# Performance work log

Hardware: AMD Instinct MI355X
Metric: run time of the kernel (lower is better)

Reference implementation:

```python
import jax, jax.numpy as jnp
import numpy as np

N_NODES = 400000
NUM_GRAPHS = 2048
IN_FEAT = 256
DENSE = 128
N_HEADS = 8


def setup_inputs() -> dict:
    key = jax.random.key(0)
    k_h, k_seg, k_w1, k_b1, k_w2, k_b2 = jax.random.split(key, 6)
    h = jax.random.normal(k_h, (N_NODES, IN_FEAT), dtype=jnp.float32)
    segment_ids = jnp.sort(
        jax.random.randint(k_seg, (N_NODES,), 0, NUM_GRAPHS, dtype=jnp.int32))
    # Linear params (jax convention: x @ W + b)
    W1 = jax.random.normal(k_w1, (IN_FEAT, DENSE), dtype=jnp.float32) / np.sqrt(IN_FEAT)
    b1 = jax.random.normal(k_b1, (DENSE,), dtype=jnp.float32) * 0.01
    W2 = jax.random.normal(k_w2, (DENSE, N_HEADS), dtype=jnp.float32) / np.sqrt(DENSE)
    b2 = jax.random.normal(k_b2, (N_HEADS,), dtype=jnp.float32) * 0.01
    return {"h": h, "segment_ids": segment_ids, "W1": W1, "b1": b1,
            "W2": W2, "b2": b2, "num_graphs": NUM_GRAPHS}


def reference(h, segment_ids, W1, b1, W2, b2, num_graphs):
    # scores: fc2(tanh(fc1(h))) -> [N, n_heads]
    scores = jnp.tanh(h @ W1 + b1) @ W2 + b2
    # ragged (per-graph) softmax over nodes, per head (dgl.softmax_nodes)
    seg_max = jax.ops.segment_max(scores, segment_ids, num_segments=num_graphs)  # [G, H]
    ex = jnp.exp(scores - seg_max[segment_ids])                                  # [N, H]
    denom = jax.ops.segment_sum(ex, segment_ids, num_segments=num_graphs)        # [G, H]
    attn = ex / denom[segment_ids]                                               # [N, H]
    # mean over heads of per-head weighted segment sums == segment sum with
    # head-averaged weights (linearity), avoiding H separate ndata passes.
    w = attn.mean(axis=1)                                                         # [N]
    out = jax.ops.segment_sum(h * w[:, None], segment_ids, num_segments=num_graphs)  # [G, in_feat]
    return out
```

## Files before the change

kernel.cpp:

```cpp
#include <hip/hip_runtime.h>
#include <hip/hip_bf16.h>

#define IN_FEAT 256
#define DENSE   128
#define NHEADS  8
#define MAXN    328
#define LDA     264
#define LDT2    136

typedef __attribute__((ext_vector_type(8))) short bf16x8_t;
typedef __attribute__((ext_vector_type(4))) float f32x4_t;

__device__ __forceinline__ unsigned int f2bf(float f) {
  unsigned int u = __float_as_uint(f);
  u += 0x7fffu + ((u >> 16) & 1u);
  return u >> 16;
}

__device__ __forceinline__ unsigned int f2bf_hu(float f) {
  return (__float_as_uint(f) + 0x8000u) >> 16;
}

__device__ __forceinline__ float fast_tanh(float x) {
  float ax = fabsf(x);
  float e = __expf(-2.0f * ax);
  float t = (1.0f - e) / (1.0f + e);
  return copysignf(t, x);
}

__global__ void seg_offsets_kernel(const int* __restrict__ seg, int* __restrict__ offs,
                                   int N, int G) {
  int i = blockIdx.x * blockDim.x + threadIdx.x;
  if (i >= N) return;
  int s  = seg[i];
  int sp = (i == 0) ? -1 : seg[i - 1];
  for (int g = sp + 1; g <= s; ++g) offs[g] = i;
  if (i == N - 1) {
    for (int g = s + 1; g <= G; ++g) offs[g] = N;
  }
}

__global__ void w1_frag_kernel(const float* __restrict__ W1, unsigned int* __restrict__ w1f) {
  int t = blockIdx.x * blockDim.x + threadIdx.x;
  if (t >= 4096) return;
  int lane = t & 63;
  int fid  = t >> 6;
  int ct = fid & 1;
  int ks = (fid >> 1) & 7;
  int wv = fid >> 4;
  int col = wv * 32 + ct * 16 + (lane & 15);
  int k0  = ks * 32 + (lane >> 4) * 8;
  unsigned int p[4];
  #pragma unroll
  for (int jj = 0; jj < 4; ++jj) {
    unsigned int lo = f2bf(W1[(size_t)(k0 + 2 * jj) * DENSE + col]);
    unsigned int hi = f2bf(W1[(size_t)(k0 + 2 * jj + 1) * DENSE + col]);
    p[jj] = lo | (hi << 16);
  }
  *(uint4*)&w1f[(size_t)t * 4] = make_uint4(p[0], p[1], p[2], p[3]);
}

__global__ void w2_frag_kernel(const float* __restrict__ W2, unsigned int* __restrict__ w2f) {
  int t = threadIdx.x;
  if (t >= 256) return;
  int lane = t & 63, ks = t >> 6;
  int hd = lane & 15, q = lane >> 4;
  unsigned int p[4];
  #pragma unroll
  for (int jj = 0; jj < 4; ++jj) {
    int k0 = ks * 32 + q * 8 + 2 * jj;
    unsigned int lo = (hd < 8) ? f2bf(W2[k0 * NHEADS + hd]) : 0u;
    unsigned int hi = (hd < 8) ? f2bf(W2[(k0 + 1) * NHEADS + hd]) : 0u;
    p[jj] = lo | (hi << 16);
  }
  *(uint4*)&w2f[(size_t)t * 4] = make_uint4(p[0], p[1], p[2], p[3]);
}

__device__ __forceinline__ int lower_bound_dev(const int* __restrict__ seg, int N, int v) {
  int lo = 0, hi = N;
  while (lo < hi) {
    int mid = (lo + hi) >> 1;
    if (seg[mid] < v) lo = mid + 1; else hi = mid;
  }
  return lo;
}

__launch_bounds__(256, 3)
__global__ void scores_kernel(const float* __restrict__ h,
                              const unsigned int* __restrict__ w1f,
                              const unsigned int* __restrict__ w2f,
                              const float* __restrict__ b1,
                              const float* __restrict__ b2,
                              float* __restrict__ scores,
                              int N) {
  __shared__ short sU[64 * LDA];
  __shared__ float sB1[DENSE];
  __shared__ float sB2[NHEADS];

  const int tid  = threadIdx.x;
  const int row0 = blockIdx.x * 64;
  const int rem  = N - row0;
  const int mcnt = rem < 64 ? rem : 64;

  const int lane = tid & 63;
  const int wv   = tid >> 6;
  const int lr   = lane & 15;
  const int q    = lane >> 4;
  const int q8   = q * 8;
  const int pfr  = tid >> 6;
  const int pfc4 = (tid & 63) * 4;

  if (tid < DENSE)  sB1[tid] = b1[tid];
  if (tid < NHEADS) sB2[tid] = b2[tid];

  short* sA = sU;
  #pragma unroll
  for (int it = 0; it < 16; ++it) {
    int row = it * 4 + pfr;
    float4 v = make_float4(0.f, 0.f, 0.f, 0.f);
    if (row < mcnt) v = *(const float4*)(h + (size_t)(row0 + row) * IN_FEAT + pfc4);
    unsigned int p0 = f2bf_hu(v.x) | (f2bf_hu(v.y) << 16);
    unsigned int p1 = f2bf_hu(v.z) | (f2bf_hu(v.w) << 16);
    *(uint2*)&sA[row * LDA + pfc4] = make_uint2(p0, p1);
  }
  __syncthreads();

  f32x4_t acc[4][2];
  #pragma unroll
  for (int mt = 0; mt < 4; ++mt) {
    acc[mt][0] = (f32x4_t){0, 0, 0, 0};
    acc[mt][1] = (f32x4_t){0, 0, 0, 0};
  }
  const bf16x8_t* w1fv = (const bf16x8_t*)w1f;
  #pragma unroll
  for (int ks = 0; ks < 8; ++ks) {
    bf16x8_t a0 = *(const bf16x8_t*)&sA[( 0 + lr) * LDA + ks * 32 + q8];
    bf16x8_t a1 = *(const bf16x8_t*)&sA[(16 + lr) * LDA + ks * 32 + q8];
    bf16x8_t a2 = *(const bf16x8_t*)&sA[(32 + lr) * LDA + ks * 32 + q8];
    bf16x8_t a3 = *(const bf16x8_t*)&sA[(48 + lr) * LDA + ks * 32 + q8];
    int f0 = ((wv * 8 + ks) * 2) * 64 + lane;
    bf16x8_t wf0 = w1fv[f0];
    bf16x8_t wf1 = w1fv[f0 + 64];
    acc[0][0] = __builtin_amdgcn_mfma_f32_16x16x32_bf16(a0, wf0, acc[0][0], 0, 0, 0);
    acc[0][1] = __builtin_amdgcn_mfma_f32_16x16x32_bf16(a0, wf1, acc[0][1], 0, 0, 0);
    acc[1][0] = __builtin_amdgcn_mfma_f32_16x16x32_bf16(a1, wf0, acc[1][0], 0, 0, 0);
    acc[1][1] = __builtin_amdgcn_mfma_f32_16x16x32_bf16(a1, wf1, acc[1][1], 0, 0, 0);
    acc[2][0] = __builtin_amdgcn_mfma_f32_16x16x32_bf16(a2, wf0, acc[2][0], 0, 0, 0);
    acc[2][1] = __builtin_amdgcn_mfma_f32_16x16x32_bf16(a2, wf1, acc[2][1], 0, 0, 0);
    acc[3][0] = __builtin_amdgcn_mfma_f32_16x16x32_bf16(a3, wf0, acc[3][0], 0, 0, 0);
    acc[3][1] = __builtin_amdgcn_mfma_f32_16x16x32_bf16(a3, wf1, acc[3][1], 0, 0, 0);
  }

  {
    float bias0 = sB1[wv * 32 + lr];
    float bias1 = sB1[wv * 32 + 16 + lr];
    #pragma unroll
    for (int mt = 0; mt < 4; ++mt)
      #pragma unroll
      for (int r = 0; r < 4; ++r) {
        acc[mt][0][r] = fast_tanh(acc[mt][0][r] + bias0);
        acc[mt][1][r] = fast_tanh(acc[mt][1][r] + bias1);
      }
  }
  __syncthreads();

  short* sTb = sU;
  #pragma unroll
  for (int mt = 0; mt < 4; ++mt) {
    int rbase = mt * 16 + q * 4;
    #pragma unroll
    for (int r = 0; r < 4; ++r) {
      sTb[(rbase + r) * LDT2 + wv * 32 + lr]      = (short)f2bf(acc[mt][0][r]);
      sTb[(rbase + r) * LDT2 + wv * 32 + 16 + lr] = (short)f2bf(acc[mt][1][r]);
    }
  }
  __syncthreads();

  {
    const bf16x8_t* w2fv = (const bf16x8_t*)w2f;
    float bias = (lr < 8) ? sB2[lr] : 0.0f;
    f32x4_t c = {bias, bias, bias, bias};
    #pragma unroll
    for (int ks = 0; ks < 4; ++ks) {
      bf16x8_t at = *(const bf16x8_t*)&sTb[(wv * 16 + lr) * LDT2 + ks * 32 + q8];
      bf16x8_t wf = w2fv[ks * 64 + lane];
      c = __builtin_amdgcn_mfma_f32_16x16x32_bf16(at, wf, c, 0, 0, 0);
    }
    #pragma unroll
    for (int r = 0; r < 4; ++r) {
      int ridx = wv * 16 + q * 4 + r;
      if (lr < 8 && ridx < mcnt)
        scores[(size_t)(row0 + ridx) * NHEADS + lr] = c[r];
    }
  }
}

__launch_bounds__(256, 4)
__global__ void pool_kernel(const float* __restrict__ h,
                            const float* __restrict__ scores,
                            const int* __restrict__ seg,
                            const int* __restrict__ offs,
                            float* __restrict__ out,
                            int N) {
  __shared__ float sS[MAXN * NHEADS];
  __shared__ float sWgt[MAXN];
  __shared__ float sRed[256];
  __shared__ float sMax[NHEADS];
  __shared__ float sInvD[NHEADS];

  const int g   = blockIdx.x;
  const int tid = threadIdx.x;

  int start, end;
  if (offs != nullptr) {
    start = offs[g];
    end   = offs[g + 1];
  } else {
    start = lower_bound_dev(seg, N, g);
    end   = lower_bound_dev(seg, N, g + 1);
  }
  int n = end - start;
  if (n > MAXN) n = MAXN;

  if (n == 0) {
    out[(size_t)g * IN_FEAT + tid] = 0.0f;
    return;
  }

  {
    const float4* sp = (const float4*)(scores + (size_t)start * NHEADS);
    float4* dp = (float4*)sS;
    int nf4 = n * 2;
    for (int idx = tid; idx < nf4; idx += 256) dp[idx] = sp[idx];
  }
  __syncthreads();

  {
    const int hd = tid & 7, ch = tid >> 3;
    float m = -3.4e38f;
    for (int i = ch; i < n; i += 32) m = fmaxf(m, sS[i * NHEADS + hd]);
    sRed[tid] = m;
    __syncthreads();
    if (tid < NHEADS) {
      float mm = sRed[tid];
      #pragma unroll
      for (int j = 1; j < 32; ++j) mm = fmaxf(mm, sRed[j * 8 + tid]);
      sMax[tid] = mm;
    }
    __syncthreads();
    float mm = sMax[hd], ssum = 0.f;
    for (int i = ch; i < n; i += 32) {
      float e = __expf(sS[i * NHEADS + hd] - mm);
      sS[i * NHEADS + hd] = e;
      ssum += e;
    }
    sRed[tid] = ssum;
    __syncthreads();
    if (tid < NHEADS) {
      float d = 0.f;
      #pragma unroll
      for (int j = 0; j < 32; ++j) d += sRed[j * 8 + tid];
      sInvD[tid] = 1.0f / d;
    }
    __syncthreads();
    for (int i = tid; i < n; i += 256) {
      float w = 0.f;
      #pragma unroll
      for (int hd2 = 0; hd2 < NHEADS; ++hd2) w += sS[i * NHEADS + hd2] * sInvD[hd2];
      sWgt[i] = 0.125f * w;
    }
    __syncthreads();
  }

  {
    const float* hp = h + (size_t)start * IN_FEAT + tid;
    float a0 = 0.f, a1 = 0.f, a2 = 0.f, a3 = 0.f;
    int i = 0;
    for (; i + 4 <= n; i += 4) {
      a0 = fmaf(sWgt[i    ], hp[(size_t)(i    ) * IN_FEAT], a0);
      a1 = fmaf(sWgt[i + 1], hp[(size_t)(i + 1) * IN_FEAT], a1);
      a2 = fmaf(sWgt[i + 2], hp[(size_t)(i + 2) * IN_FEAT], a2);
      a3 = fmaf(sWgt[i + 3], hp[(size_t)(i + 3) * IN_FEAT], a3);
    }
    for (; i < n; ++i) a0 = fmaf(sWgt[i], hp[(size_t)i * IN_FEAT], a0);
    out[(size_t)g * IN_FEAT + tid] = (a0 + a1) + (a2 + a3);
  }
}

__launch_bounds__(256, 3)
__global__ void attn_pool_fused(const float* __restrict__ h,
                                const int* __restrict__ seg,
                                const int* __restrict__ offs,
                                const float* __restrict__ W1,
                                const float* __restrict__ b1,
                                const float* __restrict__ W2,
                                const float* __restrict__ b2,
                                float* __restrict__ out,
                                int N) {
  __shared__ short sA[64 * LDA];
  __shared__ float sScores[MAXN * NHEADS];
  __shared__ float sWgt[MAXN];
  __shared__ float sW2T[NHEADS * 132];
  __shared__ float sB1[DENSE];
  __shared__ float sB2[NHEADS];
  __shared__ float sRed[256];
  __shared__ float sMax[NHEADS];
  __shared__ float sInvD[NHEADS];

  const int g   = blockIdx.x;
  const int tid = threadIdx.x;

  int start, end;
  if (offs != nullptr) { start = offs[g]; end = offs[g + 1]; }
  else { start = lower_bound_dev(seg, N, g); end = lower_bound_dev(seg, N, g + 1); }
  int n = end - start;
  if (n > MAXN) n = MAXN;
  float* sT = (float*)sA;

  if (n == 0) {
    if (tid < IN_FEAT) out[(size_t)g * IN_FEAT + tid] = 0.0f;
    return;
  }

  for (int idx = tid; idx < DENSE * NHEADS; idx += 256) {
    int k = idx >> 3; int hd = idx & 7;
    sW2T[hd * 132 + k] = W2[idx];
  }
  if (tid < DENSE)  sB1[tid] = b1[tid];
  if (tid < NHEADS) sB2[tid] = b2[tid];

  const int lane = tid & 63;
  const int wv   = tid >> 6;
  const int lr   = lane & 15;
  const int q    = lane >> 4;
  bf16x8_t b1f[16];
  #pragma unroll
  for (int ct = 0; ct < 2; ++ct) {
    int colb = wv * 32 + ct * 16 + lr;
    #pragma unroll
    for (int ks = 0; ks < 8; ++ks) {
      bf16x8_t bb;
      #pragma unroll
      for (int j = 0; j < 8; ++j)
        bb[j] = (short)f2bf(W1[(ks * 32 + q * 8 + j) * DENSE + colb]);
      b1f[ct * 8 + ks] = bb;
    }
  }

  const int ntiles = (n + 63) >> 6;
  for (int t = 0; t < ntiles; ++t) {
    const int m0   = start + t * 64;
    const int rem  = n - t * 64;
    const int mcnt = rem < 64 ? rem : 64;
    __syncthreads();
    #pragma unroll
    for (int it = 0; it < 16; ++it) {
      int row = it * 4 + (tid >> 6);
      int f4  = tid & 63;
      float4 v = make_float4(0.f, 0.f, 0.f, 0.f);
      if (row < mcnt) v = *(const float4*)(h + (size_t)(m0 + row) * IN_FEAT + f4 * 4);
      unsigned int p0 = f2bf(v.x) | (f2bf(v.y) << 16);
      unsigned int p1 = f2bf(v.z) | (f2bf(v.w) << 16);
      *(uint2*)&sA[row * LDA + f4 * 4] = make_uint2(p0, p1);
    }
    __syncthreads();
    f32x4_t acc[4][2];
    #pragma unroll
    for (int mt = 0; mt < 4; ++mt) {
      acc[mt][0] = (f32x4_t){0, 0, 0, 0};
      acc[mt][1] = (f32x4_t){0, 0, 0, 0};
    }
    #pragma unroll
    for (int ks = 0; ks < 8; ++ks) {
      bf16x8_t a0 = *(const bf16x8_t*)&sA[( 0 + lr) * LDA + ks * 32 + q * 8];
      bf16x8_t a1 = *(const bf16x8_t*)&sA[(16 + lr) * LDA + ks * 32 + q * 8];
      bf16x8_t a2 = *(const bf16x8_t*)&sA[(32 + lr) * LDA + ks * 32 + q * 8];
      bf16x8_t a3 = *(const bf16x8_t*)&sA[(48 + lr) * LDA + ks * 32 + q * 8];
      acc[0][0] = __builtin_amdgcn_mfma_f32_16x16x32_bf16(a0, b1f[ks],     acc[0][0], 0, 0, 0);
      acc[0][1] = __builtin_amdgcn_mfma_f32_16x16x32_bf16(a0, b1f[8 + ks], acc[0][1], 0, 0, 0);
      acc[1][0] = __builtin_amdgcn_mfma_f32_16x16x32_bf16(a1, b1f[ks],     acc[1][0], 0, 0, 0);
      acc[1][1] = __builtin_amdgcn_mfma_f32_16x16x32_bf16(a1, b1f[8 + ks], acc[1][1], 0, 0, 0);
      acc[2][0] = __builtin_amdgcn_mfma_f32_16x16x32_bf16(a2, b1f[ks],     acc[2][0], 0, 0, 0);
      acc[2][1] = __builtin_amdgcn_mfma_f32_16x16x32_bf16(a2, b1f[8 + ks], acc[2][1], 0, 0, 0);
      acc[3][0] = __builtin_amdgcn_mfma_f32_16x16x32_bf16(a3, b1f[ks],     acc[3][0], 0, 0, 0);
      acc[3][1] = __builtin_amdgcn_mfma_f32_16x16x32_bf16(a3, b1f[8 + ks], acc[3][1], 0, 0, 0);
    }
    __syncthreads();
    #pragma unroll
    for (int mt = 0; mt < 4; ++mt) {
      int rbase = mt * 16 + q * 4;
      #pragma unroll
      for (int ct = 0; ct < 2; ++ct) {
        int col = wv * 32 + ct * 16 + lr;
        float bias = sB1[col];
        #pragma unroll
        for (int r = 0; r < 4; ++r)
          sT[(rbase + r) * 132 + col] = fast_tanh(acc[mt][ct][r] + bias);
      }
    }
    __syncthreads();
    {
      int i0 = tid >> 3;
      int hd = tid & 7;
      #pragma unroll
      for (int half = 0; half < 2; ++half) {
        int i = i0 + half * 32;
        if (i < mcnt) {
          float s = sB2[hd];
          #pragma unroll
          for (int k4 = 0; k4 < DENSE; k4 += 4) {
            float4 tv  = *(const float4*)&sT[i * 132 + k4];
            float4 wv2 = *(const float4*)&sW2T[hd * 132 + k4];
            s = fmaf(tv.x, wv2.x, s); s = fmaf(tv.y, wv2.y, s);
            s = fmaf(tv.z, wv2.z, s); s = fmaf(tv.w, wv2.w, s);
          }
          sScores[(t * 64 + i) * NHEADS + hd] = s;
        }
      }
    }
  }
  __syncthreads();

  {
    const int hd = tid & 7, ch = tid >> 3;
    float m = -3.4e38f;
    for (int i = ch; i < n; i += 32) m = fmaxf(m, sScores[i * NHEADS + hd]);
    sRed[tid] = m;
    __syncthreads();
    if (tid < NHEADS) {
      float mm = sRed[tid];
      #pragma unroll
      for (int j = 1; j < 32; ++j) mm = fmaxf(mm, sRed[j * 8 + tid]);
      sMax[tid] = mm;
    }
    __syncthreads();
    float mm = sMax[hd], ssum = 0.f;
    for (int i = ch; i < n; i += 32) {
      float e = __expf(sScores[i * NHEADS + hd] - mm);
      sScores[i * NHEADS + hd] = e;
      ssum += e;
    }
    sRed[tid] = ssum;
    __syncthreads();
    if (tid < NHEADS) {
      float d = 0.f;
      #pragma unroll
      for (int j = 0; j < 32; ++j) d += sRed[j * 8 + tid];
      sInvD[tid] = 1.0f / d;
    }
    __syncthreads();
    for (int i = tid; i < n; i += 256) {
      float w = 0.f;
      #pragma unroll
      for (int hd2 = 0; hd2 < NHEADS; ++hd2) w += sScores[i * NHEADS + hd2] * sInvD[hd2];
      sWgt[i] = 0.125f * w;
    }
    __syncthreads();
  }

  {
    int grp = tid >> 6;
    int c4  = lane << 2;
    float4 acc = make_float4(0.f, 0.f, 0.f, 0.f);
    for (int i = grp; i < n; i += 4) {
      float w = sWgt[i];
      float4 hv = *(const float4*)(h + (size_t)(start + i) * IN_FEAT + c4);
      acc.x = fmaf(w, hv.x, acc.x);
      acc.y = fmaf(w, hv.y, acc.y);
      acc.z = fmaf(w, hv.z, acc.z);
      acc.w = fmaf(w, hv.w, acc.w);
    }
    float* sPart = (float*)sA;
    *(float4*)&sPart[grp * IN_FEAT + c4] = acc;
    __syncthreads();
    {
      float o = 0.f;
      #pragma unroll
      for (int p = 0; p < 4; ++p) o += sPart[p * IN_FEAT + tid];
      out[(size_t)g * IN_FEAT + tid] = o;
    }
  }
}

extern "C" void kernel_launch(void* const* d_in, const int* in_sizes, int n_in,
                              void* d_out, int out_size, void* d_ws, size_t ws_size,
                              hipStream_t stream) {
  const float* h   = (const float*)d_in[0];
  const int*   seg = (const int*)d_in[1];
  const float* W1  = (const float*)d_in[2];
  const float* b1v = (const float*)d_in[3];
  const float* W2  = (const float*)d_in[4];
  const float* b2v = (const float*)d_in[5];
  float* out = (float*)d_out;
  const int N = in_sizes[0] / IN_FEAT;
  const int G = out_size / IN_FEAT;

  const size_t offs_bytes  = (size_t)(G + 1) * sizeof(int);
  const size_t w1f_off     = (offs_bytes + 255) & ~(size_t)255;
  const size_t w1f_bytes   = 4096 * 16;
  const size_t w2f_off     = w1f_off + w1f_bytes;
  const size_t w2f_bytes   = 256 * 16;
  const size_t scores_off  = (w2f_off + w2f_bytes + 255) & ~(size_t)255;
  const size_t scores_bytes= (size_t)N * NHEADS * sizeof(float);

  int* offs = nullptr;
  if (ws_size >= offs_bytes) {
    offs = (int*)d_ws;
    seg_offsets_kernel<<<(N + 255) / 256, 256, 0, stream>>>(seg, offs, N, G);
  }

  if (ws_size >= scores_off + scores_bytes) {
    unsigned int* w1f = (unsigned int*)((char*)d_ws + w1f_off);
    unsigned int* w2f = (unsigned int*)((char*)d_ws + w2f_off);
    float* scores = (float*)((char*)d_ws + scores_off);
    w1_frag_kernel<<<16, 256, 0, stream>>>(W1, w1f);
    w2_frag_kernel<<<1, 256, 0, stream>>>(W2, w2f);
    scores_kernel<<<(N + 63) / 64, 256, 0, stream>>>(h, w1f, w2f, b1v, b2v, scores, N);
    pool_kernel<<<G, 256, 0, stream>>>(h, scores, seg, offs, out, N);
  } else {
    attn_pool_fused<<<G, 256, 0, stream>>>(h, seg, offs, W1, b1v, W2, b2v, out, N);
  }
}
```

Measured before the change: 198.4 us.

## Fuse score computation and pooling into one pass with atomic segment accumulation

Replaces the separate scores and per-graph pool kernels with one kernel over 32-row tiles. Each tile computes the MLP scores, exponentiates them without subtracting the segment max, and accumulates per-head exp-weighted sums of the bf16-staged h rows into a global [G,H,F] buffer and a per-head denominator buffer using atomics. A small finalize kernel then normalises and averages over heads. The aim is to read h from HBM only once instead of twice. The cost is a memset of the accumulators, many float atomics, pooling on bf16-rounded h, and reliance on scores being small enough that exp does not overflow.

```diff
diff --git a/kernel.cpp b/kernel.cpp
--- a/kernel.cpp
+++ b/kernel.cpp
@@ -5,6 +5,7 @@
 #define DENSE   128
 #define NHEADS  8
 #define MAXN    328
+#define TILE    32
 #define LDA     264
 #define LDT2    136
 
@@ -19,6 +20,10 @@
 
 __device__ __forceinline__ unsigned int f2bf_hu(float f) {
   return (__float_as_uint(f) + 0x8000u) >> 16;
+}
+
+__device__ __forceinline__ float bf2f(short s) {
+  return __uint_as_float(((unsigned int)(unsigned short)s) << 16);
 }
 
 __device__ __forceinline__ float fast_tanh(float x) {
@@ -26,18 +31,6 @@
   float e = __expf(-2.0f * ax);
   float t = (1.0f - e) / (1.0f + e);
   return copysignf(t, x);
-}
-
-__global__ void seg_offsets_kernel(const int* __restrict__ seg, int* __restrict__ offs,
-                                   int N, int G) {
-  int i = blockIdx.x * blockDim.x + threadIdx.x;
-  if (i >= N) return;
-  int s  = seg[i];
-  int sp = (i == 0) ? -1 : seg[i - 1];
-  for (int g = sp + 1; g <= s; ++g) offs[g] = i;
-  if (i == N - 1) {
-    for (int g = s + 1; g <= G; ++g) offs[g] = N;
-  }
 }
 
 __global__ void w1_frag_kernel(const float* __restrict__ W1, unsigned int* __restrict__ w1f) {
@@ -86,21 +79,26 @@
 }
 
 __launch_bounds__(256, 3)
-__global__ void scores_kernel(const float* __restrict__ h,
-                              const unsigned int* __restrict__ w1f,
-                              const unsigned int* __restrict__ w2f,
-                              const float* __restrict__ b1,
-                              const float* __restrict__ b2,
-                              float* __restrict__ scores,
-                              int N) {
-  __shared__ short sU[64 * LDA];
+__global__ void scorepool_kernel(const float* __restrict__ h,
+                                 const int* __restrict__ seg,
+                                 const unsigned int* __restrict__ w1f,
+                                 const unsigned int* __restrict__ w2f,
+                                 const float* __restrict__ b1,
+                                 const float* __restrict__ b2,
+                                 float* __restrict__ S,
+                                 float* __restrict__ D,
+                                 int N) {
+  __shared__ short sA[TILE * LDA];
+  __shared__ short sTb[TILE * LDT2];
+  __shared__ float sEx[TILE * NHEADS];
+  __shared__ int   sSeg[TILE];
   __shared__ float sB1[DENSE];
   __shared__ float sB2[NHEADS];
 
   const int tid  = threadIdx.x;
-  const int row0 = blockIdx.x * 64;
+  const int row0 = blockIdx.x * TILE;
   const int rem  = N - row0;
-  const int mcnt = rem < 64 ? rem : 64;
+  const int mcnt = rem < TILE ? rem : TILE;
 
   const int lane = tid & 63;
   const int wv   = tid >> 6;
@@ -112,10 +110,14 @@
 
   if (tid < DENSE)  sB1[tid] = b1[tid];
   if (tid < NHEADS) sB2[tid] = b2[tid];
-
-  short* sA = sU;
+  if (tid < TILE) {
+    int r = row0 + tid;
+    int rlast = row0 + mcnt - 1;
+    sSeg[tid] = seg[r <= rlast ? r : rlast];
+  }
+
   #pragma unroll
-  for (int it = 0; it < 16; ++it) {
+  for (int it = 0; it < 8; ++it) {
     int row = it * 4 + pfr;
     float4 v = make_float4(0.f, 0.f, 0.f, 0.f);
     if (row < mcnt) v = *(const float4*)(h + (size_t)(row0 + row) * IN_FEAT + pfc4);
@@ -125,58 +127,42 @@
   }
   __syncthreads();
 
-  f32x4_t acc[4][2];
-  #pragma unroll
-  for (int mt = 0; mt < 4; ++mt) {
-    acc[mt][0] = (f32x4_t){0, 0, 0, 0};
-    acc[mt][1] = (f32x4_t){0, 0, 0, 0};
-  }
-  const bf16x8_t* w1fv = (const bf16x8_t*)w1f;
-  #pragma unroll
-  for (int ks = 0; ks < 8; ++ks) {
-    bf16x8_t a0 = *(const bf16x8_t*)&sA[( 0 + lr) * LDA + ks * 32 + q8];
-    bf16x8_t a1 = *(const bf16x8_t*)&sA[(16 + lr) * LDA + ks * 32 + q8];
-    bf16x8_t a2 = *(const bf16x8_t*)&sA[(32 + lr) * LDA + ks * 32 + q8];
-    bf16x8_t a3 = *(const bf16x8_t*)&sA[(48 + lr) * LDA + ks * 32 + q8];
-    int f0 = ((wv * 8 + ks) * 2) * 64 + lane;
-    bf16x8_t wf0 = w1fv[f0];
-    bf16x8_t wf1 = w1fv[f0 + 64];
-    acc[0][0] = __builtin_amdgcn_mfma_f32_16x16x32_bf16(a0, wf0, acc[0][0], 0, 0, 0);
-    acc[0][1] = __builtin_amdgcn_mfma_f32_16x16x32_bf16(a0, wf1, acc[0][1], 0, 0, 0);
-    acc[1][0] = __builtin_amdgcn_mfma_f32_16x16x32_bf16(a1, wf0, acc[1][0], 0, 0, 0);
-    acc[1][1] = __builtin_amdgcn_mfma_f32_16x16x32_bf16(a1, wf1, acc[1][1], 0, 0, 0);
-    acc[2][0] = __builtin_amdgcn_mfma_f32_16x16x32_bf16(a2, wf0, acc[2][0], 0, 0, 0);
-    acc[2][1] = __builtin_amdgcn_mfma_f32_16x16x32_bf16(a2, wf1, acc[2][1], 0, 0, 0);
-    acc[3][0] = __builtin_amdgcn_mfma_f32_16x16x32_bf16(a3, wf0, acc[3][0], 0, 0, 0);
-    acc[3][1] = __builtin_amdgcn_mfma_f32_16x16x32_bf16(a3, wf1, acc[3][1], 0, 0, 0);
-  }
-
   {
+    f32x4_t a00 = {0,0,0,0}, a01 = {0,0,0,0}, a10 = {0,0,0,0}, a11 = {0,0,0,0};
+    const bf16x8_t* w1fv = (const bf16x8_t*)w1f;
+    #pragma unroll
+    for (int ks = 0; ks < 8; ++ks) {
+      bf16x8_t av0 = *(const bf16x8_t*)&sA[(     lr) * LDA + ks * 32 + q8];
+      bf16x8_t av1 = *(const bf16x8_t*)&sA[(16 + lr) * LDA + ks * 32 + q8];
+      int f0 = ((wv * 8 + ks) * 2) * 64 + lane;
+      bf16x8_t wf0 = w1fv[f0];
+      bf16x8_t wf1 = w1fv[f0 + 64];
+      a00 = __builtin_amdgcn_mfma_f32_16x16x32_bf16(av0, wf0, a00, 0, 0, 0);
+      a01 = __builtin_amdgcn_mfma_f32_16x16x32_bf16(av0, wf1, a01, 0, 0, 0);
+      a10 = __builtin_amdgcn_mfma_f32_16x16x32_bf16(av1, wf0, a10, 0, 0, 0);
+      a11 = __builtin_amdgcn_mfma_f32_16x16x32_bf16(av1, wf1, a11, 0, 0, 0);
+    }
     float bias0 = sB1[wv * 32 + lr];
     float bias1 = sB1[wv * 32 + 16 + lr];
     #pragma unroll
-    for (int mt = 0; mt < 4; ++mt)
-      #pragma unroll
-      for (int r = 0; r < 4; ++r) {
-        acc[mt][0][r] = fast_tanh(acc[mt][0][r] + bias0);
-        acc[mt][1][r] = fast_tanh(acc[mt][1][r] + bias1);
-      }
+    for (int r = 0; r < 4; ++r) {
+      a00[r] = fast_tanh(a00[r] + bias0);
+      a01[r] = fast_tanh(a01[r] + bias1);
+      a10[r] = fast_tanh(a10[r] + bias0);
+      a11[r] = fast_tanh(a11[r] + bias1);
+    }
+    #pragma unroll
+    for (int r = 0; r < 4; ++r) {
+      int row0r = q * 4 + r, row1r = 16 + q * 4 + r;
+      sTb[row0r * LDT2 + wv * 32 + lr]      = (short)f2bf(a00[r]);
+      sTb[row0r * LDT2 + wv * 32 + 16 + lr] = (short)f2bf(a01[r]);
+      sTb[row1r * LDT2 + wv * 32 + lr]      = (short)f2bf(a10[r]);
+      sTb[row1r * LDT2 + wv * 32 + 16 + lr] = (short)f2bf(a11[r]);
+    }
   }
   __syncthreads();
 
-  short* sTb = sU;
-  #pragma unroll
-  for (int mt = 0; mt < 4; ++mt) {
-    int rbase = mt * 16 + q * 4;
-    #pragma unroll
-    for (int r = 0; r < 4; ++r) {
-      sTb[(rbase + r) * LDT2 + wv * 32 + lr]      = (short)f2bf(acc[mt][0][r]);
-      sTb[(rbase + r) * LDT2 + wv * 32 + 16 + lr] = (short)f2bf(acc[mt][1][r]);
-    }
-  }
-  __syncthreads();
-
-  {
+  if (wv < 2) {
     const bf16x8_t* w2fv = (const bf16x8_t*)w2f;
     float bias = (lr < 8) ? sB2[lr] : 0.0f;
     f32x4_t c = {bias, bias, bias, bias};
@@ -189,108 +175,76 @@
     #pragma unroll
     for (int r = 0; r < 4; ++r) {
       int ridx = wv * 16 + q * 4 + r;
-      if (lr < 8 && ridx < mcnt)
-        scores[(size_t)(row0 + ridx) * NHEADS + lr] = c[r];
-    }
-  }
-}
-
-__launch_bounds__(256, 4)
-__global__ void pool_kernel(const float* __restrict__ h,
-                            const float* __restrict__ scores,
-                            const int* __restrict__ seg,
-                            const int* __restrict__ offs,
-                            float* __restrict__ out,
-                            int N) {
-  __shared__ float sS[MAXN * NHEADS];
-  __shared__ float sWgt[MAXN];
-  __shared__ float sRed[256];
-  __shared__ float sMax[NHEADS];
-  __shared__ float sInvD[NHEADS];
-
-  const int g   = blockIdx.x;
-  const int tid = threadIdx.x;
-
-  int start, end;
-  if (offs != nullptr) {
-    start = offs[g];
-    end   = offs[g + 1];
-  } else {
-    start = lower_bound_dev(seg, N, g);
-    end   = lower_bound_dev(seg, N, g + 1);
-  }
-  int n = end - start;
-  if (n > MAXN) n = MAXN;
-
-  if (n == 0) {
-    out[(size_t)g * IN_FEAT + tid] = 0.0f;
-    return;
-  }
+      if (lr < 8) sEx[ridx * NHEADS + lr] = (ridx < mcnt) ? __expf(c[r]) : 0.0f;
+    }
+  }
+  __syncthreads();
 
   {
-    const float4* sp = (const float4*)(scores + (size_t)start * NHEADS);
-    float4* dp = (float4*)sS;
-    int nf4 = n * 2;
-    for (int idx = tid; idx < nf4; idx += 256) dp[idx] = sp[idx];
+    const int c = tid;
+    float acc[NHEADS];
+    #pragma unroll
+    for (int hh = 0; hh < NHEADS; ++hh) acc[hh] = 0.f;
+    int curg = sSeg[0];
+    for (int i = 0; i < TILE; ++i) {
+      int gi = sSeg[i];
+      if (gi != curg) {
+        #pragma unroll
+        for (int hh = 0; hh < NHEADS; ++hh) {
+          unsafeAtomicAdd(&S[((size_t)curg * NHEADS + hh) * IN_FEAT + c], acc[hh]);
+          acc[hh] = 0.f;
+        }
+        curg = gi;
+      }
+      float hv = bf2f(sA[i * LDA + c]);
+      float4 e0 = *(const float4*)&sEx[i * NHEADS];
+      float4 e1 = *(const float4*)&sEx[i * NHEADS + 4];
+      acc[0] = fmaf(e0.x, hv, acc[0]); acc[1] = fmaf(e0.y, hv, acc[1]);
+      acc[2] = fmaf(e0.z, hv, acc[2]); acc[3] = fmaf(e0.w, hv, acc[3]);
+      acc[4] = fmaf(e1.x, hv, acc[4]); acc[5] = fmaf(e1.y, hv, acc[5]);
+      acc[6] = fmaf(e1.z, hv, acc[6]); acc[7] = fmaf(e1.w, hv, acc[7]);
+    }
+    #pragma unroll
+    for (int hh = 0; hh < NHEADS; ++hh)
+      unsafeAtomicAdd(&S[((size_t)curg * NHEADS + hh) * IN_FEAT + c], acc[hh]);
+  }
+
+  if (tid < NHEADS) {
+    const int hh = tid;
+    float d = 0.f;
+    int curg = sSeg[0];
+    for (int i = 0; i < TILE; ++i) {
+      int gi = sSeg[i];
+      if (gi != curg) {
+        unsafeAtomicAdd(&D[(size_t)curg * NHEADS + hh], d);
+        d = 0.f; curg = gi;
+      }
+      d += sEx[i * NHEADS + hh];
+    }
+    unsafeAtomicAdd(&D[(size_t)curg * NHEADS + hh], d);
+  }
+}
+
+__global__ void finalize_kernel(const float* __restrict__ S,
+                                const float* __restrict__ D,
+                                float* __restrict__ out) {
+  __shared__ float sInv[NHEADS];
+  const int g = blockIdx.x, c = threadIdx.x;
+  if (c < NHEADS) {
+    float d = D[(size_t)g * NHEADS + c];
+    sInv[c] = (d > 0.f) ? (1.0f / d) : 0.f;
   }
   __syncthreads();
-
-  {
-    const int hd = tid & 7, ch = tid >> 3;
-    float m = -3.4e38f;
-    for (int i = ch; i < n; i += 32) m = fmaxf(m, sS[i * NHEADS + hd]);
-    sRed[tid] = m;
-    __syncthreads();
-    if (tid < NHEADS) {
-      float mm = sRed[tid];
-      #pragma unroll
-      for (int j = 1; j < 32; ++j) mm = fmaxf(mm, sRed[j * 8 + tid]);
-      sMax[tid] = mm;
-    }
-    __syncthreads();
-    float mm = sMax[hd], ssum = 0.f;
-    for (int i = ch; i < n; i += 32) {
-      float e = __expf(sS[i * NHEADS + hd] - mm);
-      sS[i * NHEADS + hd] = e;
-      ssum += e;
-    }
-    sRed[tid] = ssum;
-    __syncthreads();
-    if (tid < NHEADS) {
-      float d = 0.f;
-      #pragma unroll
-      for (int j = 0; j < 32; ++j) d += sRed[j * 8 + tid];
-      sInvD[tid] = 1.0f / d;
-    }
-    __syncthreads();
-    for (int i = tid; i < n; i += 256) {
-      float w = 0.f;
-      #pragma unroll
-      for (int hd2 = 0; hd2 < NHEADS; ++hd2) w += sS[i * NHEADS + hd2] * sInvD[hd2];
-      sWgt[i] = 0.125f * w;
-    }
-    __syncthreads();
-  }
-
-  {
-    const float* hp = h + (size_t)start * IN_FEAT + tid;
-    float a0 = 0.f, a1 = 0.f, a2 = 0.f, a3 = 0.f;
-    int i = 0;
-    for (; i + 4 <= n; i += 4) {
-      a0 = fmaf(sWgt[i    ], hp[(size_t)(i    ) * IN_FEAT], a0);
-      a1 = fmaf(sWgt[i + 1], hp[(size_t)(i + 1) * IN_FEAT], a1);
-      a2 = fmaf(sWgt[i + 2], hp[(size_t)(i + 2) * IN_FEAT], a2);
-      a3 = fmaf(sWgt[i + 3], hp[(size_t)(i + 3) * IN_FEAT], a3);
-    }
-    for (; i < n; ++i) a0 = fmaf(sWgt[i], hp[(size_t)i * IN_FEAT], a0);
-    out[(size_t)g * IN_FEAT + tid] = (a0 + a1) + (a2 + a3);
-  }
+  float s = 0.f;
+  #pragma unroll
+  for (int hh = 0; hh < NHEADS; ++hh)
+    s = fmaf(S[((size_t)g * NHEADS + hh) * IN_FEAT + c], sInv[hh], s);
+  out[(size_t)g * IN_FEAT + c] = 0.125f * s;
 }
 
 __launch_bounds__(256, 3)
 __global__ void attn_pool_fused(const float* __restrict__ h,
                                 const int* __restrict__ seg,
-                                const int* __restrict__ offs,
                                 const float* __restrict__ W1,
                                 const float* __restrict__ b1,
                                 const float* __restrict__ W2,
@@ -310,9 +264,8 @@
   const int g   = blockIdx.x;
   const int tid = threadIdx.x;
 
-  int start, end;
-  if (offs != nullptr) { start = offs[g]; end = offs[g + 1]; }
-  else { start = lower_bound_dev(seg, N, g); end = lower_bound_dev(seg, N, g + 1); }
+  int start = lower_bound_dev(seg, N, g);
+  int end   = lower_bound_dev(seg, N, g + 1);
   int n = end - start;
   if (n > MAXN) n = MAXN;
   float* sT = (float*)sA;
@@ -495,29 +448,25 @@
   const int N = in_sizes[0] / IN_FEAT;
   const int G = out_size / IN_FEAT;
 
-  const size_t offs_bytes  = (size_t)(G + 1) * sizeof(int);
-  const size_t w1f_off     = (offs_bytes + 255) & ~(size_t)255;
-  const size_t w1f_bytes   = 4096 * 16;
-  const size_t w2f_off     = w1f_off + w1f_bytes;
-  const size_t w2f_bytes   = 256 * 16;
-  const size_t scores_off  = (w2f_off + w2f_bytes + 255) & ~(size_t)255;
-  const size_t scores_bytes= (size_t)N * NHEADS * sizeof(float);
-
-  int* offs = nullptr;
-  if (ws_size >= offs_bytes) {
-    offs = (int*)d_ws;
-    seg_offsets_kernel<<<(N + 255) / 256, 256, 0, stream>>>(seg, offs, N, G);
-  }
-
-  if (ws_size >= scores_off + scores_bytes) {
-    unsigned int* w1f = (unsigned int*)((char*)d_ws + w1f_off);
-    unsigned int* w2f = (unsigned int*)((char*)d_ws + w2f_off);
-    float* scores = (float*)((char*)d_ws + scores_off);
+  const size_t w1f_bytes = 4096 * 16;
+  const size_t w2f_bytes = 256 * 16;
+  const size_t S_off   = (w1f_bytes + w2f_bytes + 255) & ~(size_t)255;
+  const size_t S_bytes = (size_t)G * NHEADS * IN_FEAT * sizeof(float);
+  const size_t D_off   = S_off + S_bytes;
+  const size_t D_bytes = (size_t)G * NHEADS * sizeof(float);
+
+  if (ws_size >= D_off + D_bytes) {
+    unsigned int* w1f = (unsigned int*)d_ws;
+    unsigned int* w2f = (unsigned int*)((char*)d_ws + w1f_bytes);
+    float* S  = (float*)((char*)d_ws + S_off);
+    float* Dp = (float*)((char*)d_ws + D_off);
+    hipMemsetAsync((char*)d_ws + S_off, 0, S_bytes + D_bytes, stream);
     w1_frag_kernel<<<16, 256, 0, stream>>>(W1, w1f);
     w2_frag_kernel<<<1, 256, 0, stream>>>(W2, w2f);
-    scores_kernel<<<(N + 63) / 64, 256, 0, stream>>>(h, w1f, w2f, b1v, b2v, scores, N);
-    pool_kernel<<<G, 256, 0, stream>>>(h, scores, seg, offs, out, N);
+    scorepool_kernel<<<(N + TILE - 1) / TILE, 256, 0, stream>>>(
+        h, seg, w1f, w2f, b1v, b2v, S, Dp, N);
+    finalize_kernel<<<G, 256, 0, stream>>>(S, Dp, out);
   } else {
-    attn_pool_fused<<<G, 256, 0, stream>>>(h, seg, offs, W1, b1v, W2, b2v, out, N);
-  }
-}
+    attn_pool_fused<<<G, 256, 0, stream>>>(h, seg, W1, b1v, W2, b2v, out, N);
+  }
+}
```

New measurement: 223.0 us. 12.4% more time.
